# Performance work log

Hardware: AMD Instinct MI355X
Metric: run time of the kernel (lower is better)

## Reference

```python
import jax, jax.numpy as jnp
import numpy as np

X_DIM = 64
Y_DIM = 64
U_DIM = 64
BATCH = 32
SEQ_LEN = 2048
DT = 1.0 / 1024.0
EPS = 1e-4


def setup_inputs() -> dict:
    key = jax.random.key(0)
    k_y, k_a, k_c = jax.random.split(key, 3)
    y = jax.random.normal(k_y, (BATCH, SEQ_LEN, Y_DIM), dtype=jnp.float32)
    # parameters, matching the module's initialization (small noise added to A/C for generality)
    A = jnp.diag(-0.01 * (jnp.arange(X_DIM, dtype=jnp.float32) + 1.0)) \
        + 0.001 * jax.random.normal(k_a, (X_DIM, X_DIM), dtype=jnp.float32)
    B = jnp.eye(X_DIM, U_DIM, dtype=jnp.float32) * 0.1
    C = 0.1 * jax.random.normal(k_c, (Y_DIM, X_DIM), dtype=jnp.float32)
    L_Q = jnp.eye(X_DIM, dtype=jnp.float32) * 0.316
    L_R = jnp.eye(U_DIM, dtype=jnp.float32) * 0.316
    L_V = jnp.eye(Y_DIM, dtype=jnp.float32)
    L_Q_proc = jnp.eye(X_DIM, dtype=jnp.float32) * 0.1
    x0_mean = jnp.zeros((X_DIM,), dtype=jnp.float32)
    P0 = jnp.eye(X_DIM, dtype=jnp.float32) * 0.1
    return {"y": y, "A": A, "B": B, "C": C, "L_Q": L_Q, "L_R": L_R,
            "L_V": L_V, "L_Q_proc": L_Q_proc, "x0_mean": x0_mean, "P0": P0}


def _riccati_step(S, H, n):
    # Euler step of the augmented Hamiltonian flow; P = V @ U^{-1}
    S_new = S + DT * (H @ S)
    U, V = S_new[:n], S_new[n:]
    X = V @ jnp.linalg.inv(U)
    return X, S_new


def _forward(y, A, B, C, L_Q, L_R, L_V, L_Q_proc, x0_mean, P0):
    n = A.shape[0]
    u_dim = B.shape[1]
    y_dim = C.shape[0]
    batch, seq_len, _ = y.shape

    Q = L_Q @ L_Q.T
    R = L_R @ L_R.T
    V = L_V @ L_V.T
    Q_proc = L_Q_proc @ L_Q_proc.T

    # normalize observations (torch.std is unbiased -> ddof=1)
    y_mean = y.mean(axis=(0, 1), keepdims=True)
    y_std = y.std(axis=(0, 1), keepdims=True, ddof=1)
    yn = (y - y_mean) / (y_std + EPS)

    # --- LQR Riccati recursion: P_seq, K_seq (sequential scan over time) ---
    R_inv_reg = jnp.linalg.inv(R + EPS * jnp.eye(u_dim, dtype=R.dtype))
    H_care = jnp.block([[A, -B @ jnp.linalg.inv(R) @ B.T],
                        [-Q, -A.T]])  # augmented Hamiltonian (2n, 2n)

    def lqr_step(S, _):
        X, S_new = _riccati_step(S, H_care, n)
        P = 0.5 * (X + X.T)
        K = R_inv_reg @ (B.T @ P)  # (u_dim, n)
        return S_new, (P, K)

    S0 = jnp.concatenate([jnp.eye(n, dtype=Q.dtype), Q], axis=0)  # P0 = Q
    _, (P_seq, K_seq) = jax.lax.scan(lqr_step, S0, None, length=seq_len)

    # --- Kalman filter (sequential scan, data-dependent per-step linear algebra) ---
    V_reg = V + EPS * jnp.eye(y_dim, dtype=V.dtype)
    V_chol = jnp.linalg.cholesky(V_reg)
    log_det_V = 2.0 * jnp.sum(jnp.log(jnp.diagonal(V_chol)))
    Z = jnp.zeros((n, n), dtype=A.dtype)
    LOG_2PI = jnp.log(2.0 * jnp.pi).astype(A.dtype)

    def kf_step(carry, inp):
        x_t, S, ll = carry
        K_t, y_t = inp  # (u_dim, n), (batch, y_dim)
        A_eff = A - B @ K_t
        x_pred = x_t + DT * (x_t @ A_eff.T)  # (batch, n)
        H_t = jnp.block([[A_eff, Q_proc], [Z, -A_eff.T]])
        P_new, S = _riccati_step(S, H_t, n)
        P_pred = 0.5 * (P_new + P_new.T)
        residual = y_t - x_pred @ C.T  # (batch, y_dim)
        CtP = C @ P_pred  # (y_dim, n)
        Sm = CtP @ C.T + V
        S_inv = jnp.linalg.inv(Sm + EPS * jnp.eye(y_dim, dtype=Sm.dtype))
        Kg = CtP.T @ S_inv  # (n, y_dim)
        x_new = x_pred + residual @ Kg.T
        quad = jnp.sum(residual * (residual @ S_inv.T))  # sum_b r^T S_inv r
        ll = ll - 0.5 * (quad + log_det_V + y_dim * LOG_2PI)
        return (x_new, S, ll), x_new

    S0_kf = jnp.concatenate([jnp.eye(n, dtype=P0.dtype), P0], axis=0)
    x0 = jnp.broadcast_to(x0_mean, (batch, n))
    y_t_major = jnp.swapaxes(yn, 0, 1)  # (T, B, y_dim)
    (_, _, ll), x_filt_t = jax.lax.scan(kf_step, (x0, S0_kf, jnp.float32(0.0)),
                                        (K_seq, y_t_major))
    x_filt = jnp.swapaxes(x_filt_t, 0, 1)  # (B, T, n)
    log_likelihood = ll / seq_len

    # controls, prediction, quadratic costs (fully vectorized)
    u_seq = -jnp.einsum('tux,btx->btu', K_seq, x_filt)
    y_pred = x_filt @ C.T
    x_cost = jnp.einsum('btx,xz,btz->b', x_filt, Q, x_filt)
    u_cost = jnp.einsum('btu,uv,btv->b', u_seq, R, u_seq)
    control_cost = jnp.mean(x_cost + u_cost)
    return log_likelihood, control_cost, x_filt, u_seq, y_pred, yn


def reference(y, A, B, C, L_Q, L_R, L_V, L_Q_proc, x0_mean, P0):
    return _forward(y, A, B, C, L_Q, L_R, L_V, L_Q_proc, x0_mean, P0)
```

## Files before the change

kernel.cpp:

```cpp
#include <hip/hip_runtime.h>
#include <math.h>

#define XD 64
#define SEQL 2048
#define NB 32
#define DT_C  (1.0f/1024.0f)
#define EPS_C 1e-4f
#define LD 68
#define PLD 136
#define LOG2PI 1.8378770664093453f
#define CHUNK 16
#define NCH 128

#define OFF_PARTIAL 0u
#define OFF_MEAN    32768u
#define OFF_STD     32832u
#define OFF_Q       32896u
#define OFF_R       36992u
#define OFF_VM      41088u
#define OFF_QP      45184u
#define OFF_RIREG   49280u
#define OFF_LOGDET  53376u
#define OFF_CHAIN   53440u
#define OFF_POW     250048u
#define OFF_BOUNDS  1298624u
#define OFF_K       1568960u
#define OFF_AEFF    9957568u
#define OFF_UV      18346176u
#define OFF_G       35123392u
#define OFF_B       43512000u
#define OFF_OPS2    47706304u
#define OFF_OPS3G   50852032u
#define OFF_OPS3B   51900608u
#define OFF_SB2     52424896u
#define OFF_XB      53473472u
#define OFF_QUAD    53735616u
#define OFF_COST    53737664u

#define OOFF_XF 2
#define OOFF_U  4194306
#define OOFF_YP 8388610
#define OOFF_YN 12582914

template<int KD>
__device__ __forceinline__ void mmNN(int t, float* __restrict__ out, int ldo,
    const float* __restrict__ A, int lda, const float* __restrict__ B, int ldb,
    const float* __restrict__ addC = nullptr, int ldc = 0, float alpha = 1.0f)
{
  const int r0 = (t >> 4) << 2, c0 = (t & 15) << 2;
  float acc[4][4] = {};
  for (int k = 0; k < KD; k += 4) {
    float a_[4][4];
    #pragma unroll
    for (int i = 0; i < 4; ++i) {
      const float4 x = *(const float4*)&A[(r0+i)*lda + k];
      a_[i][0]=x.x; a_[i][1]=x.y; a_[i][2]=x.z; a_[i][3]=x.w;
    }
    #pragma unroll
    for (int kk = 0; kk < 4; ++kk) {
      const float4 bv = *(const float4*)&B[(k+kk)*ldb + c0];
      #pragma unroll
      for (int i = 0; i < 4; ++i) {
        const float a = a_[i][kk];
        acc[i][0] += a*bv.x; acc[i][1] += a*bv.y; acc[i][2] += a*bv.z; acc[i][3] += a*bv.w;
      }
    }
  }
  #pragma unroll
  for (int i = 0; i < 4; ++i)
    #pragma unroll
    for (int j = 0; j < 4; ++j) {
      float v = alpha*acc[i][j];
      if (addC) v += addC[(r0+i)*ldc + (c0+j)];
      out[(r0+i)*ldo + (c0+j)] = v;
    }
}

template<int KD>
__device__ __forceinline__ void mmTA(int t, float* __restrict__ out, int ldo,
    const float* __restrict__ A, int lda, const float* __restrict__ B, int ldb,
    const float* __restrict__ addC = nullptr, int ldc = 0, float alpha = 1.0f)
{
  const int r0 = (t >> 4) << 2, c0 = (t & 15) << 2;
  float acc[4][4] = {};
  for (int k = 0; k < KD; k += 4) {
    #pragma unroll
    for (int kk = 0; kk < 4; ++kk) {
      const float4 av4 = *(const float4*)&A[(k+kk)*lda + r0];
      const float4 bv4 = *(const float4*)&B[(k+kk)*ldb + c0];
      const float av[4] = {av4.x, av4.y, av4.z, av4.w};
      const float bv[4] = {bv4.x, bv4.y, bv4.z, bv4.w};
      #pragma unroll
      for (int i = 0; i < 4; ++i)
        #pragma unroll
        for (int j = 0; j < 4; ++j)
          acc[i][j] += av[i]*bv[j];
    }
  }
  #pragma unroll
  for (int i = 0; i < 4; ++i)
    #pragma unroll
    for (int j = 0; j < 4; ++j) {
      float v = alpha*acc[i][j];
      if (addC) v += addC[(r0+i)*ldc + (c0+j)];
      out[(r0+i)*ldo + (c0+j)] = v;
    }
}

template<int KD>
__device__ __forceinline__ void mmTB(int t, float* __restrict__ out, int ldo,
    const float* __restrict__ A, int lda, const float* __restrict__ B, int ldb,
    const float* __restrict__ addC = nullptr, int ldc = 0, float alpha = 1.0f)
{
  const int r0 = (t >> 4) << 2, c0 = (t & 15) << 2;
  float acc[4][4] = {};
  for (int k = 0; k < KD; k += 4) {
    float a_[4][4], b_[4][4];
    #pragma unroll
    for (int i = 0; i < 4; ++i) {
      const float4 x = *(const float4*)&A[(r0+i)*lda + k];
      a_[i][0]=x.x; a_[i][1]=x.y; a_[i][2]=x.z; a_[i][3]=x.w;
    }
    #pragma unroll
    for (int j = 0; j < 4; ++j) {
      const float4 x = *(const float4*)&B[(c0+j)*ldb + k];
      b_[j][0]=x.x; b_[j][1]=x.y; b_[j][2]=x.z; b_[j][3]=x.w;
    }
    #pragma unroll
    for (int i = 0; i < 4; ++i)
      #pragma unroll
      for (int j = 0; j < 4; ++j)
        acc[i][j] += a_[i][0]*b_[j][0] + a_[i][1]*b_[j][1] + a_[i][2]*b_[j][2] + a_[i][3]*b_[j][3];
  }
  #pragma unroll
  for (int i = 0; i < 4; ++i)
    #pragma unroll
    for (int j = 0; j < 4; ++j) {
      float v = alpha*acc[i][j];
      if (addC) v += addC[(r0+i)*ldc + (c0+j)];
      out[(r0+i)*ldo + (c0+j)] = v;
    }
}

template<int KD>
__device__ __forceinline__ void mm32NN(int t, float* __restrict__ out, int ldo,
    const float* __restrict__ A, int lda, const float* __restrict__ B, int ldb,
    const float* __restrict__ addC = nullptr, int ldc = 0, float alpha = 1.0f)
{
  const int r0 = (t >> 4) << 1, c0 = (t & 15) << 2;
  float acc[2][4] = {};
  for (int k = 0; k < KD; k += 4) {
    float a_[2][4];
    #pragma unroll
    for (int i = 0; i < 2; ++i) {
      const float4 x = *(const float4*)&A[(r0+i)*lda + k];
      a_[i][0]=x.x; a_[i][1]=x.y; a_[i][2]=x.z; a_[i][3]=x.w;
    }
    #pragma unroll
    for (int kk = 0; kk < 4; ++kk) {
      const float4 bv = *(const float4*)&B[(k+kk)*ldb + c0];
      #pragma unroll
      for (int i = 0; i < 2; ++i) {
        const float a = a_[i][kk];
        acc[i][0] += a*bv.x; acc[i][1] += a*bv.y; acc[i][2] += a*bv.z; acc[i][3] += a*bv.w;
      }
    }
  }
  #pragma unroll
  for (int i = 0; i < 2; ++i)
    #pragma unroll
    for (int j = 0; j < 4; ++j) {
      float v = alpha*acc[i][j];
      if (addC) v += addC[(r0+i)*ldc + (c0+j)];
      out[(r0+i)*ldo + (c0+j)] = v;
    }
}

template<int KD>
__device__ __forceinline__ void mm32TB(int t, float* __restrict__ out, int ldo,
    const float* __restrict__ A, int lda, const float* __restrict__ B, int ldb,
    const float* __restrict__ addC = nullptr, int ldc = 0, float alpha = 1.0f)
{
  const int r0 = (t >> 4) << 1, c0 = (t & 15) << 2;
  float acc[2][4] = {};
  for (int k = 0; k < KD; k += 4) {
    float a_[2][4], b_[4][4];
    #pragma unroll
    for (int i = 0; i < 2; ++i) {
      const float4 x = *(const float4*)&A[(r0+i)*lda + k];
      a_[i][0]=x.x; a_[i][1]=x.y; a_[i][2]=x.z; a_[i][3]=x.w;
    }
    #pragma unroll
    for (int j = 0; j < 4; ++j) {
      const float4 x = *(const float4*)&B[(c0+j)*ldb + k];
      b_[j][0]=x.x; b_[j][1]=x.y; b_[j][2]=x.z; b_[j][3]=x.w;
    }
    #pragma unroll
    for (int i = 0; i < 2; ++i)
      #pragma unroll
      for (int j = 0; j < 4; ++j)
        acc[i][j] += a_[i][0]*b_[j][0] + a_[i][1]*b_[j][1] + a_[i][2]*b_[j][2] + a_[i][3]*b_[j][3];
  }
  #pragma unroll
  for (int i = 0; i < 2; ++i)
    #pragma unroll
    for (int j = 0; j < 4; ++j) {
      float v = alpha*acc[i][j];
      if (addC) v += addC[(r0+i)*ldc + (c0+j)];
      out[(r0+i)*ldo + (c0+j)] = v;
    }
}

__device__ __forceinline__ void gj64(int t, float* __restrict__ Am, float* __restrict__ R)
{
  const int r = t >> 2;
  const int c0 = (t & 3) << 4;
  for (int k = 0; k < 64; ++k) {
    __syncthreads();
    const float pv = Am[k*LD + k];
    const float f = Am[r*LD + k] / pv;
    if (r != k) {
      #pragma unroll
      for (int c = 0; c < 16; c += 4) {
        float4 ak = *(const float4*)&Am[k*LD + c0 + c];
        float4 ar = *(float4*)&Am[r*LD + c0 + c];
        ar.x -= f*ak.x; ar.y -= f*ak.y; ar.z -= f*ak.z; ar.w -= f*ak.w;
        *(float4*)&Am[r*LD + c0 + c] = ar;
        float4 rk = *(const float4*)&R[k*LD + c0 + c];
        float4 rr = *(float4*)&R[r*LD + c0 + c];
        rr.x -= f*rk.x; rr.y -= f*rk.y; rr.z -= f*rk.z; rr.w -= f*rk.w;
        *(float4*)&R[r*LD + c0 + c] = rr;
      }
    }
  }
  __syncthreads();
  const float dinv = 1.0f / Am[r*LD + r];
  #pragma unroll
  for (int c = 0; c < 16; c += 4) {
    float4 rr = *(float4*)&R[r*LD + c0 + c];
    rr.x *= dinv; rr.y *= dinv; rr.z *= dinv; rr.w *= dinv;
    *(float4*)&R[r*LD + c0 + c] = rr;
  }
  __syncthreads();
}

__device__ __forceinline__ void gjb8(int t, float* __restrict__ Am, float* __restrict__ R,
                                     float* __restrict__ pnl, float* __restrict__ w8)
{
  const int r  = t >> 2;
  const int c0 = (t & 3) << 4;
  const int j2 = t >> 5;
  const int cc = (t & 31) << 2;
  for (int kb = 0; kb < 8; ++kb) {
    const int K = kb << 3;
    __syncthreads();
    if (t < 64) {
      const int i = t >> 3, j = t & 7;
      float a = Am[(K+i)*LD + K + j];
      float w = (i == j) ? 1.0f : 0.0f;
      #pragma unroll
      for (int p = 0; p < 8; ++p) {
        const float pv  = __shfl(a, p*8 + p, 64);
        const float aip = __shfl(a, i*8 + p, 64);
        const float apj = __shfl(a, p*8 + j, 64);
        const float wpj = __shfl(w, p*8 + j, 64);
        const float fi  = aip / pv;
        if (i == p) { a = a / pv; w = w / pv; }
        else        { a -= fi * apj; w -= fi * wpj; }
      }
      w8[t] = w;
    }
    __syncthreads();
    {
      const int c4 = cc & 63;
      const float* srcB = (cc < 64) ? Am : R;
      const int off = (cc < 64) ? 0 : 68;
      float4 acc = make_float4(0.f, 0.f, 0.f, 0.f);
      #pragma unroll
      for (int m = 0; m < 8; ++m) {
        const float wv = w8[j2*8 + m];
        const float4 rv = *(const float4*)&srcB[(K+m)*LD + c4];
        acc.x += wv*rv.x; acc.y += wv*rv.y; acc.z += wv*rv.z; acc.w += wv*rv.w;
      }
      *(float4*)&pnl[j2*PLD + off + c4] = acc;
    }
    __syncthreads();
    {
      const float4 f0 = *(const float4*)&Am[r*LD + K];
      const float4 f1 = *(const float4*)&Am[r*LD + K + 4];
      const float fj[8] = {f0.x, f0.y, f0.z, f0.w, f1.x, f1.y, f1.z, f1.w};
      const bool inK = ((unsigned)(r - K)) < 8u;
      #pragma unroll
      for (int c = 0; c < 16; c += 4) {
        const int cab = c0 + c;
        if (cab >= K + 8) {
          float4 v;
          if (inK) {
            v = *(const float4*)&pnl[(r-K)*PLD + cab];
          } else {
            v = *(float4*)&Am[r*LD + cab];
            #pragma unroll
            for (int j = 0; j < 8; ++j) {
              const float4 p4 = *(const float4*)&pnl[j*PLD + cab];
              v.x -= fj[j]*p4.x; v.y -= fj[j]*p4.y; v.z -= fj[j]*p4.z; v.w -= fj[j]*p4.w;
            }
          }
          *(float4*)&Am[r*LD + cab] = v;
        }
      }
      #pragma unroll
      for (int c = 0; c < 16; c += 4) {
        const int cab = c0 + c;
        float4 v;
        if (inK) {
          v = *(const float4*)&pnl[(r-K)*PLD + 68 + cab];
        } else {
          v = *(float4*)&R[r*LD + cab];
          #pragma unroll
          for (int j = 0; j < 8; ++j) {
            const float4 p4 = *(const float4*)&pnl[j*PLD + 68 + cab];
            v.x -= fj[j]*p4.x; v.y -= fj[j]*p4.y; v.z -= fj[j]*p4.z; v.w -= fj[j]*p4.w;
          }
        }
        *(float4*)&R[r*LD + cab] = v;
      }
    }
  }
  __syncthreads();
}


__global__ __launch_bounds__(256) void k_stats(const float* __restrict__ y, float* __restrict__ ws)
{
  __shared__ float sbuf[4][128];
  const int t = threadIdx.x, blk = blockIdx.x;
  const int d = t & 63, g = t >> 6;
  float s = 0.f, s2 = 0.f;
  for (int r = g; r < 256; r += 4) {
    const float v = y[(size_t)(blk*256 + r)*64 + d];
    s += v; s2 += v*v;
  }
  sbuf[g][d] = s; sbuf[g][64+d] = s2;
  __syncthreads();
  if (t < 128) ws[OFF_PARTIAL + (size_t)blk*128 + t] = sbuf[0][t]+sbuf[1][t]+sbuf[2][t]+sbuf[3][t];
}

__global__ __launch_bounds__(256) void k_setup(
    const float* __restrict__ A, const float* __restrict__ Bi,
    const float* __restrict__ LQ, const float* __restrict__ LR,
    const float* __restrict__ LV, const float* __restrict__ LQp,
    float* __restrict__ ws)
{
  __shared__ float b1[64*LD], b2[64*LD], b3[64*LD], b4[64*LD], bQ[64*LD];
  __shared__ float sred[128];
  const int t = threadIdx.x;

  if (t < 128) {
    float acc = 0.f;
    for (int p = 0; p < 256; ++p) acc += ws[OFF_PARTIAL + (size_t)p*128 + t];
    sred[t] = acc;
  }
  __syncthreads();
  if (t < 64) {
    const float mean = sred[t] * (1.0f/65536.0f);
    const float var = (sred[64+t] - 65536.0f*mean*mean) * (1.0f/65535.0f);
    ws[OFF_MEAN + t] = mean;
    ws[OFF_STD + t] = sqrtf(var);
  }

  mmTB<64>(t, bQ, LD, LQ, 64, LQ, 64);
  mmTB<64>(t, b3, LD, LR, 64, LR, 64);
  mmTB<64>(t, ws+OFF_VM, 64, LV, 64, LV, 64);
  mmTB<64>(t, ws+OFF_QP, 64, LQp, 64, LQp, 64);
  __syncthreads();
  for (int idx = t; idx < 4096; idx += 256) {
    const int r = idx>>6, c = idx&63;
    ws[OFF_Q + idx] = bQ[r*LD+c];
    ws[OFF_R + idx] = b3[r*LD+c];
    b1[r*LD+c] = b3[r*LD+c] + ((r==c)?EPS_C:0.f);
    b2[r*LD+c] = (r==c)?1.f:0.f;
  }
  gj64(t, b1, b2);
  for (int idx = t; idx < 4096; idx += 256) ws[OFF_RIREG + idx] = b2[(idx>>6)*LD+(idx&63)];
  __syncthreads();
  for (int idx = t; idx < 4096; idx += 256) {
    const int r = idx>>6, c = idx&63;
    b1[r*LD+c] = b3[r*LD+c];
    b2[r*LD+c] = (r==c)?1.f:0.f;
  }
  gj64(t, b1, b2);
  mmTB<64>(t, b3, LD, b2, LD, Bi, 64);
  __syncthreads();
  mmNN<64>(t, b4, LD, Bi, 64, b3, LD);
  mmTB<64>(t, b1, LD, LV, 64, LV, 64);
  __syncthreads();
  if (t < 64) b1[t*LD+t] += EPS_C;
  {
    const int r = t >> 2, c0 = (t & 3) << 4;
    float lsum = 0.f;
    for (int k = 0; k < 64; ++k) {
      __syncthreads();
      const float pv = b1[k*LD+k];
      lsum += logf(pv);
      const float f = b1[r*LD+k] / pv;
      if (r != k) {
        #pragma unroll
        for (int c = 0; c < 16; c += 4) {
          float4 ak = *(const float4*)&b1[k*LD+c0+c];
          float4 ar = *(float4*)&b1[r*LD+c0+c];
          ar.x -= f*ak.x; ar.y -= f*ak.y; ar.z -= f*ak.z; ar.w -= f*ak.w;
          *(float4*)&b1[r*LD+c0+c] = ar;
        }
      }
    }
    if (t == 0) ws[OFF_LOGDET] = lsum;
  }
  __syncthreads();
  float* M0 = ws + OFF_CHAIN;
  for (int idx = t; idx < 16384; idx += 256) {
    const int i = idx >> 7, j = idx & 127;
    float v;
    if (i < 64) v = (j < 64) ? (((i==j)?1.f:0.f) + DT_C*A[i*64+j]) : (-DT_C*b4[i*LD + (j-64)]);
    else        v = (j < 64) ? (-DT_C*bQ[(i-64)*LD + j]) : (((i==j)?1.f:0.f) - DT_C*A[(j-64)*64 + (i-64)]);
    M0[idx] = v;
  }
  for (int idx = t; idx < 16384; idx += 256) {
    const int i = idx >> 7, j = idx & 127;
    ws[OFF_POW + idx] = (i==j)?1.f:0.f;
  }
  for (int idx = t; idx < 8192; idx += 256) {
    const int i = idx >> 6, j = idx & 63;
    ws[OFF_BOUNDS + idx] = (i < 64) ? ((i==j)?1.f:0.f) : bQ[(i-64)*LD + j];
  }
}

__global__ __launch_bounds__(256) void k_yn(const float* __restrict__ y, const float* __restrict__ ws, float* __restrict__ out)
{
  const size_t i0 = ((size_t)blockIdx.x*256 + threadIdx.x)*4;
  const int d = (int)(i0 & 63);
  const float4 v = *(const float4*)&y[i0];
  const float4 m = *(const float4*)&ws[OFF_MEAN + d];
  const float4 s = *(const float4*)&ws[OFF_STD + d];
  float* o = out + OOFF_YN + i0;
  o[0] = (v.x - m.x)/(s.x + EPS_C);
  o[1] = (v.y - m.y)/(s.y + EPS_C);
  o[2] = (v.z - m.z)/(s.z + EPS_C);
  o[3] = (v.w - m.w)/(s.w + EPS_C);
}

__global__ __launch_bounds__(256) void k_sq(const float* __restrict__ src, float* __restrict__ dst)
{
  const int t = threadIdx.x;
  const int r = blockIdx.x*8 + (t >> 5);
  const int c0 = (t & 31) << 2;
  float acc[4] = {0.f,0.f,0.f,0.f};
  for (int k = 0; k < 128; k += 4) {
    const float4 a4 = *(const float4*)&src[r*128 + k];
    const float av[4] = {a4.x, a4.y, a4.z, a4.w};
    #pragma unroll
    for (int kk = 0; kk < 4; ++kk) {
      const float4 bv = *(const float4*)&src[(k+kk)*128 + c0];
      acc[0] += av[kk]*bv.x; acc[1] += av[kk]*bv.y; acc[2] += av[kk]*bv.z; acc[3] += av[kk]*bv.w;
    }
  }
  float4 o; o.x=acc[0]; o.y=acc[1]; o.z=acc[2]; o.w=acc[3];
  *(float4*)&dst[r*128 + c0] = o;
}

__global__ __launch_bounds__(256) void k_pow(const float* __restrict__ chainj, float* __restrict__ powt, int level)
{
  const int i = blockIdx.x >> 2, sub = blockIdx.x & 3;
  const float* Bm = powt + (size_t)i*16384;
  float* D = powt + (size_t)(i + (1<<level))*16384;
  const int t = threadIdx.x;
  const int r0 = sub*32 + ((t >> 4) << 1);
  const int c0 = (t & 15) << 3;
  float acc[2][8] = {};
  for (int k = 0; k < 128; k += 4) {
    float a_[2][4];
    {
      const float4 x = *(const float4*)&chainj[r0*128 + k];
      a_[0][0]=x.x; a_[0][1]=x.y; a_[0][2]=x.z; a_[0][3]=x.w;
      const float4 y2 = *(const float4*)&chainj[(r0+1)*128 + k];
      a_[1][0]=y2.x; a_[1][1]=y2.y; a_[1][2]=y2.z; a_[1][3]=y2.w;
    }
    #pragma unroll
    for (int kk = 0; kk < 4; ++kk) {
      const float4 b0 = *(const float4*)&Bm[(k+kk)*128 + c0];
      const float4 b1v = *(const float4*)&Bm[(k+kk)*128 + c0 + 4];
      #pragma unroll
      for (int i2 = 0; i2 < 2; ++i2) {
        const float a = a_[i2][kk];
        acc[i2][0] += a*b0.x; acc[i2][1] += a*b0.y; acc[i2][2] += a*b0.z; acc[i2][3] += a*b0.w;
        acc[i2][4] += a*b1v.x; acc[i2][5] += a*b1v.y; acc[i2][6] += a*b1v.z; acc[i2][7] += a*b1v.w;
      }
    }
  }
  #pragma unroll
  for (int i2 = 0; i2 < 2; ++i2)
    #pragma unroll
    for (int j = 0; j < 8; ++j)
      D[(r0+i2)*128 + c0 + j] = acc[i2][j];
}

__global__ __launch_bounds__(256) void k_boundsk(const float* __restrict__ chainp, float* __restrict__ ws, int level)
{
  const int kb = blockIdx.x >> 1, sub = blockIdx.x & 1;
  const int dsti = kb + (1 << level);
  if (dsti > 32) return;
  const float* S = ws + OFF_BOUNDS + (size_t)kb*8192;
  float* D = ws + OFF_BOUNDS + (size_t)dsti*8192;
  const int t = threadIdx.x;
  const int r0 = sub*64 + ((t >> 4) << 2);
  const int c0 = (t & 15) << 2;
  float acc[4][4] = {};
  for (int k = 0; k < 128; k += 4) {
    float a_[4][4];
    #pragma unroll
    for (int i = 0; i < 4; ++i) {
      const float4 x = *(const float4*)&chainp[(r0+i)*128 + k];
      a_[i][0]=x.x; a_[i][1]=x.y; a_[i][2]=x.z; a_[i][3]=x.w;
    }
    #pragma unroll
    for (int kk = 0; kk < 4; ++kk) {
      const float4 bv = *(const float4*)&S[(k+kk)*64 + c0];
      #pragma unroll
      for (int i = 0; i < 4; ++i) {
        const float a = a_[i][kk];
        acc[i][0] += a*bv.x; acc[i][1] += a*bv.y; acc[i][2] += a*bv.z; acc[i][3] += a*bv.w;
      }
    }
  }
  #pragma unroll
  for (int i = 0; i < 4; ++i)
    #pragma unroll
    for (int j = 0; j < 4; ++j)
      D[(r0+i)*64 + c0 + j] = acc[i][j];
}

__global__ __launch_bounds__(256) void k_lqr(const float* __restrict__ Ain, const float* __restrict__ Bin, float* __restrict__ ws)
{
  __shared__ float b1[64*LD], b2[64*LD], b3[64*LD];
  __shared__ float pnl[8*PLD], w8[64];
  const int t = threadIdx.x, tt = blockIdx.x;
  const int tp1 = tt + 1, kc = tp1 >> 6, rr = tp1 & 63;
  const float* Mr = ws + OFF_POW + (size_t)rr*16384;
  const float* SB = ws + OFF_BOUNDS + (size_t)kc*8192;
  mmNN<128>(t, b1, LD, Mr, 128, SB, 64);
  mmNN<128>(t, b3, LD, Mr + 8192, 128, SB, 64);
  for (int idx = t; idx < 4096; idx += 256) {
    const int r = idx>>6, c = idx&63;
    b2[r*LD+c] = (r==c)?1.f:0.f;
  }
  gjb8(t, b1, b2, pnl, w8);
  mmNN<64>(t, b1, LD, b3, LD, b2, LD);
  __syncthreads();
  for (int idx = t; idx < 4096; idx += 256) {
    const int r = idx>>6, c = idx&63;
    b3[r*LD+c] = 0.5f*(b1[r*LD+c] + b1[c*LD+r]);
  }
  __syncthreads();
  mmTA<64>(t, b1, LD, Bin, 64, b3, LD);
  __syncthreads();
  mmNN<64>(t, b2, LD, ws+OFF_RIREG, 64, b1, LD);
  __syncthreads();
  float* Kout = ws + OFF_K + (size_t)tt*4096;
  for (int idx = t; idx < 4096; idx += 256) Kout[idx] = b2[(idx>>6)*LD+(idx&63)];
  mmNN<64>(t, b1, LD, Bin, 64, b2, LD);
  __syncthreads();
  float* Ae = ws + OFF_AEFF + (size_t)tt*4096;
  for (int idx = t; idx < 4096; idx += 256) Ae[idx] = Ain[idx] - b1[(idx>>6)*LD+(idx&63)];
}

__global__ __launch_bounds__(1024) void k_ops2(const float* __restrict__ ws_aeff, const float* __restrict__ ws_qp, float* __restrict__ dstE)
{
  __shared__ float E[64*LD], W[64*LD], F[64*LD], T1[64*LD], T2[64*LD], T3[64*LD], T4[64*LD];
  const int t = threadIdx.x, c = blockIdx.x, g = t >> 8, tl = t & 255;
  for (int idx = t; idx < 4096; idx += 1024) {
    const int r = idx>>6, cc = idx&63; const float id = (r==cc)?1.f:0.f;
    E[r*LD+cc] = id; W[r*LD+cc] = 0.f; F[r*LD+cc] = id;
  }
  __syncthreads();
  for (int s = 0; s < CHUNK; ++s) {
    const float* Ae = ws_aeff + ((size_t)c*CHUNK + s)*4096;
    if (g == 0)      mmNN<64>(tl, T1, LD, Ae, 64, E, LD);
    else if (g == 1) mmNN<64>(tl, T2, LD, Ae, 64, W, LD);
    else if (g == 2) mmNN<64>(tl, T3, LD, ws_qp, 64, F, LD);
    else             mmTA<64>(tl, T4, LD, Ae, 64, F, LD);
    __syncthreads();
    for (int idx = t; idx < 4096; idx += 1024) {
      const int p = (idx>>6)*LD + (idx&63);
      E[p] += DT_C*T1[p];
      W[p] += DT_C*(T2[p] + T3[p]);
      F[p] -= DT_C*T4[p];
    }
    __syncthreads();
  }
  float* dst = dstE + (size_t)c*12288;
  for (int idx = t; idx < 4096; idx += 1024) {
    const int p = (idx>>6)*LD + (idx&63);
    dst[idx] = E[p]; dst[4096+idx] = W[p]; dst[8192+idx] = F[p];
  }
}

__global__ __launch_bounds__(1024) void k_scan2(const float* __restrict__ src, float* __restrict__ dst, int s)
{
  __shared__ float t1[64*LD], t2[64*LD];
  const int i = blockIdx.x, t = threadIdx.x, g = t>>8, tl = t&255;
  const float* si = src + (size_t)i*12288;
  float* di = dst + (size_t)i*12288;
  if (i < s) {
    for (int idx = t; idx < 12288; idx += 1024) di[idx] = si[idx];
    return;
  }
  const float* sj = src + (size_t)(i-s)*12288;
  if (g == 0)      mmNN<64>(tl, di, 64, si, 64, sj, 64);
  else if (g == 1) mmNN<64>(tl, t1, LD, si, 64, sj+4096, 64);
  else if (g == 2) mmNN<64>(tl, t2, LD, si+4096, 64, sj+8192, 64);
  else             mmNN<64>(tl, di+8192, 64, si+8192, 64, sj+8192, 64);
  __syncthreads();
  for (int idx = t; idx < 4096; idx += 1024) {
    const int p = (idx>>6)*LD + (idx&63);
    di[4096+idx] = t1[p] + t2[p];
  }
}

__global__ __launch_bounds__(256) void k_sb2(const float* __restrict__ phi, const float* __restrict__ P0, float* __restrict__ ws)
{
  const int c = blockIdx.x, t = threadIdx.x;
  float* D = ws + OFF_SB2 + (size_t)c*8192;
  if (c == 0) {
    for (int idx = t; idx < 4096; idx += 256) {
      const int r = idx>>6, cc = idx&63;
      D[idx] = (r==cc)?1.f:0.f;
      D[4096+idx] = P0[idx];
    }
    return;
  }
  const float* ph = phi + (size_t)(c-1)*12288;
  mmNN<64>(t, D, 64, ph+4096, 64, P0, 64, ph, 64);
  mmNN<64>(t, D+4096, 64, ph+8192, 64, P0, 64);
}

__global__ __launch_bounds__(1024) void k_uvwalk(const float* __restrict__ ws_aeff, const float* __restrict__ ws_qp,
    const float* __restrict__ ws_sb2, float* __restrict__ ws_uv)
{
  __shared__ float U[64*LD], V[64*LD], T1[64*LD], T2[64*LD], T3[64*LD];
  const int c = blockIdx.x, t = threadIdx.x, g = t>>8, tl = t&255;
  const float* S = ws_sb2 + (size_t)c*8192;
  for (int idx = t; idx < 4096; idx += 1024) {
    const int p = (idx>>6)*LD + (idx&63);
    U[p] = S[idx]; V[p] = S[4096+idx];
  }
  __syncthreads();
  for (int s = 0; s < CHUNK; ++s) {
    const size_t tt = (size_t)c*CHUNK + s;
    const float* Ae = ws_aeff + tt*4096;
    if (g == 0)      mmNN<64>(tl, T1, LD, Ae, 64, U, LD);
    else if (g == 1) mmNN<64>(tl, T2, LD, ws_qp, 64, V, LD);
    else if (g == 2) mmTA<64>(tl, T3, LD, Ae, 64, V, LD);
    __syncthreads();
    float* O = ws_uv + tt*8192;
    for (int idx = t; idx < 4096; idx += 1024) {
      const int p = (idx>>6)*LD + (idx&63);
      const float un = U[p] + DT_C*(T1[p] + T2[p]);
      const float vn = V[p] - DT_C*T3[p];
      U[p] = un; V[p] = vn;
      O[idx] = un; O[4096+idx] = vn;
    }
    __syncthreads();
  }
}

__global__ __launch_bounds__(256) void k_kfper(const float* __restrict__ Cin, float* __restrict__ ws)
{
  __shared__ float b1[64*LD], b2[64*LD], b3[64*LD];
  __shared__ float pnl[8*PLD], w8[64];
  const int t = threadIdx.x, tt = blockIdx.x;
  float* base = ws + OFF_UV + (size_t)tt*8192;
  for (int idx = t; idx < 4096; idx += 256) {
    const int r = idx>>6, c = idx&63;
    b1[r*LD+c] = base[idx];
    b2[r*LD+c] = (r==c)?1.f:0.f;
  }
  gjb8(t, b1, b2, pnl, w8);
  mmNN<64>(t, b3, LD, base+4096, 64, b2, LD);
  __syncthreads();
  for (int idx = t; idx < 4096; idx += 256) {
    const int r = idx>>6, c = idx&63;
    b1[r*LD+c] = 0.5f*(b3[r*LD+c] + b3[c*LD+r]);
  }
  __syncthreads();
  mmNN<64>(t, b3, LD, Cin, 64, b1, LD);
  __syncthreads();
  mmTB<64>(t, b2, LD, b3, LD, Cin, 64, ws+OFF_VM, 64);
  __syncthreads();
  if (t < 64) b2[t*LD+t] += EPS_C;
  for (int idx = t; idx < 4096; idx += 256) {
    const int r = idx>>6, c = idx&63;
    b1[r*LD+c] = (r==c)?1.f:0.f;
  }
  gjb8(t, b2, b1, pnl, w8);
  for (int idx = t; idx < 4096; idx += 256) base[4096+idx] = b1[(idx>>6)*LD+(idx&63)];
  mmTA<64>(t, b2, LD, b3, LD, b1, LD);
  __syncthreads();
  for (int idx = t; idx < 4096; idx += 256) base[idx] = b2[(idx>>6)*LD+(idx&63)];
  mmNN<64>(t, b3, LD, b2, LD, Cin, 64);
  __syncthreads();
  const float* Ae = ws + OFF_AEFF + (size_t)tt*4096;
  float* Gg = ws + OFF_G + (size_t)tt*4096;
  {
    const int r0 = (t>>4)<<2, cg0 = (t&15)<<2;
    float acc[4][4] = {};
    for (int k = 0; k < 64; k += 4) {
      float a_[4][4];
      #pragma unroll
      for (int kk = 0; kk < 4; ++kk) {
        const float4 x = *(const float4*)&Ae[(k+kk)*64 + r0];
        a_[kk][0]=x.x; a_[kk][1]=x.y; a_[kk][2]=x.z; a_[kk][3]=x.w;
      }
      float yv[4][4];
      #pragma unroll
      for (int j = 0; j < 4; ++j) {
        const float4 z4 = *(const float4*)&b3[(cg0+j)*LD + k];
        yv[j][0] = -z4.x; yv[j][1] = -z4.y; yv[j][2] = -z4.z; yv[j][3] = -z4.w;
        const int dk = (cg0+j) - k;
        if (dk >= 0 && dk < 4) yv[j][dk] += 1.0f;
      }
      #pragma unroll
      for (int kk = 0; kk < 4; ++kk)
        #pragma unroll
        for (int i = 0; i < 4; ++i) {
          const float a = a_[kk][i];
          #pragma unroll
          for (int j = 0; j < 4; ++j) acc[i][j] += a * yv[j][kk];
        }
    }
    #pragma unroll
    for (int i = 0; i < 4; ++i)
      #pragma unroll
      for (int j = 0; j < 4; ++j) {
        const int rw = r0+i, cw = cg0+j;
        const float Yij = ((rw==cw)?1.f:0.f) - b3[cw*LD + rw];
        Gg[rw*64+cw] = Yij + DT_C*acc[i][j];
      }
  }
}

__global__ __launch_bounds__(256) void k_bvec(const float* __restrict__ outyn, float* __restrict__ ws)
{
  __shared__ float y32[NB*LD];
  const int tt = blockIdx.x, t = threadIdx.x;
  for (int idx = t; idx < 2048; idx += 256) {
    const int i = idx>>6, d = idx&63;
    y32[i*LD+d] = outyn[(size_t)i*131072 + (size_t)tt*64 + d];
  }
  __syncthreads();
  mm32TB<64>(t, ws + OFF_B + (size_t)tt*2048, 64, y32, LD, ws + OFF_UV + (size_t)tt*8192, 64);
}

__global__ __launch_bounds__(1024) void k_ops3(const float* __restrict__ ws_g, const float* __restrict__ ws_b,
    float* __restrict__ dG, float* __restrict__ dB)
{
  __shared__ float Gc[64*LD], TG[64*LD], bc[NB*LD], Tb[NB*LD];
  const int t = threadIdx.x, c = blockIdx.x, g = t >> 8, tl = t & 255;
  for (int idx = t; idx < 4096; idx += 1024) {
    const int r = idx>>6, cc = idx&63;
    Gc[r*LD+cc] = (r==cc)?1.f:0.f;
  }
  for (int idx = t; idx < 2048; idx += 1024) bc[(idx>>6)*LD+(idx&63)] = 0.f;
  __syncthreads();
  for (int s = 0; s < CHUNK; ++s) {
    const size_t tt = (size_t)c*CHUNK + s;
    const float* Gt = ws_g + tt*4096;
    if (g == 0)      mmNN<64>(tl, TG, LD, Gc, LD, Gt, 64);
    else if (g == 1) mm32NN<64>(tl, Tb, LD, bc, LD, Gt, 64);
    __syncthreads();
    for (int idx = t; idx < 4096; idx += 1024) {
      const int p = (idx>>6)*LD + (idx&63);
      Gc[p] = TG[p];
    }
    const float* bt = ws_b + tt*2048;
    for (int idx = t; idx < 2048; idx += 1024) {
      const int p = (idx>>6)*LD + (idx&63);
      bc[p] = Tb[p] + bt[idx];
    }
    __syncthreads();
  }
  for (int idx = t; idx < 4096; idx += 1024) dG[(size_t)c*4096 + idx] = Gc[(idx>>6)*LD+(idx&63)];
  for (int idx = t; idx < 2048; idx += 1024) dB[(size_t)c*2048 + idx] = bc[(idx>>6)*LD+(idx&63)];
}

__global__ __launch_bounds__(512) void k_scan3(const float* __restrict__ sG, const float* __restrict__ sB,
    float* __restrict__ dG, float* __restrict__ dB, int s)
{
  const int i = blockIdx.x, t = threadIdx.x, g = t>>8, tl = t&255;
  if (i < s) {
    for (int idx = t; idx < 4096; idx += 512) dG[(size_t)i*4096+idx] = sG[(size_t)i*4096+idx];
    for (int idx = t; idx < 2048; idx += 512) dB[(size_t)i*2048+idx] = sB[(size_t)i*2048+idx];
    return;
  }
  const float* Ge = sG + (size_t)(i-s)*4096;
  const float* Gl = sG + (size_t)i*4096;
  if (g == 0) mmNN<64>(tl, dG + (size_t)i*4096, 64, Ge, 64, Gl, 64);
  else        mm32NN<64>(tl, dB + (size_t)i*2048, 64, sB + (size_t)(i-s)*2048, 64, Gl, 64,
                         sB + (size_t)i*2048, 64);
}

__global__ __launch_bounds__(256) void k_xb(const float* __restrict__ phiG, const float* __restrict__ phiB,
    const float* __restrict__ x0, float* __restrict__ ws)
{
  __shared__ float v[64];
  const int c = blockIdx.x, t = threadIdx.x;
  float* D = ws + OFF_XB + (size_t)c*2048;
  if (c == 0) {
    for (int idx = t; idx < 2048; idx += 256) D[idx] = x0[idx&63];
    return;
  }
  const float* G = phiG + (size_t)(c-1)*4096;
  const float* b = phiB + (size_t)(c-1)*2048;
  if (t < 64) {
    float acc = 0.f;
    for (int k = 0; k < 64; ++k) acc += x0[k]*G[k*64 + t];
    v[t] = acc;
  }
  __syncthreads();
  for (int idx = t; idx < 2048; idx += 256) D[idx] = v[idx&63] + b[idx];
}

__global__ __launch_bounds__(256) void k_xwalk(const float* __restrict__ ws_g, const float* __restrict__ ws_b,
    const float* __restrict__ ws_xb, float* __restrict__ outx)
{
  __shared__ float x[NB*LD], xn[NB*LD];
  const int c = blockIdx.x, t = threadIdx.x;
  const float* X0 = ws_xb + (size_t)c*2048;
  for (int idx = t; idx < 2048; idx += 256) x[(idx>>6)*LD+(idx&63)] = X0[idx];
  __syncthreads();
  for (int s = 0; s < CHUNK; ++s) {
    const size_t tt = (size_t)c*CHUNK + s;
    mm32NN<64>(t, xn, LD, x, LD, ws_g + tt*4096, 64, ws_b + tt*2048, 64);
    __syncthreads();
    for (int idx = t; idx < 2048; idx += 256) {
      const int i = idx>>6, d = idx&63;
      const float val = xn[i*LD+d];
      x[i*LD+d] = val;
      outx[(size_t)i*131072 + tt*64 + d] = val;
    }
    __syncthreads();
  }
}

__global__ __launch_bounds__(256) void k_final(const float* __restrict__ Cin, const float* __restrict__ x0,
    const float* __restrict__ outx, const float* __restrict__ outyn,
    float* __restrict__ outu, float* __restrict__ outyp, float* __restrict__ ws)
{
  __shared__ float xc[NB*LD], z[NB*LD], t1[NB*LD], t2[NB*LD];
  __shared__ float red4[4];
  const int tt = blockIdx.x, t = threadIdx.x;
  for (int idx = t; idx < 2048; idx += 256) {
    const int i = idx>>6, d = idx&63;
    xc[i*LD+d] = outx[(size_t)i*131072 + (size_t)tt*64 + d];
    z[i*LD+d]  = (tt == 0) ? x0[d] : outx[(size_t)i*131072 + (size_t)(tt-1)*64 + d];
  }
  __syncthreads();
  mm32TB<64>(t, t1, LD, xc, LD, ws + OFF_K + (size_t)tt*4096, 64, nullptr, 0, -1.0f);
  mm32TB<64>(t, t2, LD, xc, LD, Cin, 64);
  __syncthreads();
  for (int idx = t; idx < 2048; idx += 256) {
    const int i = idx>>6, d = idx&63;
    outu[(size_t)i*131072 + (size_t)tt*64 + d]  = t1[i*LD+d];
    outyp[(size_t)i*131072 + (size_t)tt*64 + d] = t2[i*LD+d];
  }
  __syncthreads();
  mm32NN<64>(t, t2, LD, xc, LD, ws + OFF_Q, 64);
  __syncthreads();
  const int i_ = t >> 3, lane8 = t & 7;
  float cpart = 0.f;
  for (int d = lane8; d < 64; d += 8) cpart += t2[i_*LD+d]*xc[i_*LD+d];
  __syncthreads();
  mm32NN<64>(t, t2, LD, t1, LD, ws + OFF_R, 64);
  __syncthreads();
  for (int d = lane8; d < 64; d += 8) cpart += t2[i_*LD+d]*t1[i_*LD+d];
  cpart += __shfl_down(cpart, 4, 8);
  cpart += __shfl_down(cpart, 2, 8);
  cpart += __shfl_down(cpart, 1, 8);
  if (lane8 == 0) ws[OFF_COST + (size_t)tt*32 + i_] = cpart;
  __syncthreads();
  mm32TB<64>(t, t2, LD, z, LD, ws + OFF_AEFF + (size_t)tt*4096, 64, z, LD, DT_C);
  __syncthreads();
  mm32TB<64>(t, t1, LD, t2, LD, Cin, 64, outyn + (size_t)tt*64, 131072, -1.0f);
  __syncthreads();
  mm32TB<64>(t, z, LD, t1, LD, ws + OFF_UV + (size_t)tt*8192 + 4096, 64);
  __syncthreads();
  float q = 0.f;
  for (int idx = t; idx < 2048; idx += 256) {
    const int p = (idx>>6)*LD + (idx&63);
    q += t1[p]*z[p];
  }
  q += __shfl_down(q, 32); q += __shfl_down(q, 16); q += __shfl_down(q, 8);
  q += __shfl_down(q, 4);  q += __shfl_down(q, 2);  q += __shfl_down(q, 1);
  if ((t & 63) == 0) red4[t>>6] = q;
  __syncthreads();
  if (t == 0) ws[OFF_QUAD + tt] = red4[0]+red4[1]+red4[2]+red4[3];
}

__global__ __launch_bounds__(256) void k_scalars(const float* __restrict__ ws, float* __restrict__ out)
{
  __shared__ float red[256];
  const int t = threadIdx.x;
  float q = 0.f;
  for (int i = t; i < 2048; i += 256) q += ws[OFF_QUAD + i];
  red[t] = q;
  __syncthreads();
  for (int s = 128; s > 0; s >>= 1) { if (t < s) red[t] += red[t+s]; __syncthreads(); }
  const float quadsum = red[0];
  __syncthreads();
  {
    const int b = t & 31, chunk = t >> 5;
    float a = 0.f;
    for (int j = 0; j < 256; ++j) a += ws[OFF_COST + (size_t)(chunk*256 + j)*32 + b];
    red[t] = a;
  }
  __syncthreads();
  if (t < 32) {
    float a = 0.f;
    for (int ch = 0; ch < 8; ++ch) a += red[ch*32 + t];
    red[t] = a;
  }
  __syncthreads();
  if (t == 0) {
    float cc = 0.f;
    for (int b = 0; b < 32; ++b) cc += red[b];
    out[1] = cc / 32.0f;
    const float ld = ws[OFF_LOGDET];
    out[0] = -0.5f*(quadsum + 2048.0f*(ld + 64.0f*LOG2PI)) / 2048.0f;
  }
}

extern "C" void kernel_launch(void* const* d_in, const int* in_sizes, int n_in,
                              void* d_out, int out_size, void* d_ws, size_t ws_size,
                              hipStream_t stream)
{
  (void)in_sizes; (void)n_in; (void)out_size; (void)ws_size;
  const float* y   = (const float*)d_in[0];
  const float* A   = (const float*)d_in[1];
  const float* Bi  = (const float*)d_in[2];
  const float* C   = (const float*)d_in[3];
  const float* LQ  = (const float*)d_in[4];
  const float* LR  = (const float*)d_in[5];
  const float* LV  = (const float*)d_in[6];
  const float* LQp = (const float*)d_in[7];
  const float* x0  = (const float*)d_in[8];
  const float* P0  = (const float*)d_in[9];
  float* out = (float*)d_out;
  float* ws  = (float*)d_ws;

  k_stats<<<256, 256, 0, stream>>>(y, ws);
  k_setup<<<1, 256, 0, stream>>>(A, Bi, LQ, LR, LV, LQp, ws);
  k_yn<<<4096, 256, 0, stream>>>(y, ws, out);

  for (int j = 1; j <= 11; ++j)
    k_sq<<<16, 256, 0, stream>>>(ws + OFF_CHAIN + (size_t)(j-1)*16384, ws + OFF_CHAIN + (size_t)j*16384);
  for (int j = 0; j <= 5; ++j)
    k_pow<<<4 << j, 256, 0, stream>>>(ws + OFF_CHAIN + (size_t)j*16384, ws + OFF_POW, j);
  for (int j = 0; j <= 5; ++j)
    k_boundsk<<<2 << j, 256, 0, stream>>>(ws + OFF_CHAIN + (size_t)(6+j)*16384, ws, j);

  k_lqr<<<2048, 256, 0, stream>>>(A, Bi, ws);

  k_ops2<<<NCH, 1024, 0, stream>>>(ws + OFF_AEFF, ws + OFF_QP, ws + OFF_OPS2);
  {
    float* pa = ws + OFF_OPS2;
    float* pb = pa + (size_t)NCH*12288;
    float* src = pa; float* dst = pb;
    for (int s = 1; s < NCH; s <<= 1) {
      k_scan2<<<NCH, 1024, 0, stream>>>(src, dst, s);
      float* tmp = src; src = dst; dst = tmp;
    }
    k_sb2<<<NCH, 256, 0, stream>>>(src, P0, ws);
  }
  k_uvwalk<<<NCH, 1024, 0, stream>>>(ws + OFF_AEFF, ws + OFF_QP, ws + OFF_SB2, ws + OFF_UV);
  k_kfper<<<2048, 256, 0, stream>>>(C, ws);

  k_bvec<<<2048, 256, 0, stream>>>(out + OOFF_YN, ws);
  k_ops3<<<NCH, 1024, 0, stream>>>(ws + OFF_G, ws + OFF_B, ws + OFF_OPS3G, ws + OFF_OPS3B);
  {
    float* ga = ws + OFF_OPS3G; float* gb = ga + (size_t)NCH*4096;
    float* ba = ws + OFF_OPS3B; float* bb = ba + (size_t)NCH*2048;
    float *gs = ga, *gd = gb, *bs = ba, *bd = bb;
    for (int s = 1; s < NCH; s <<= 1) {
      k_scan3<<<NCH, 512, 0, stream>>>(gs, bs, gd, bd, s);
      float* t1p = gs; gs = gd; gd = t1p;
      float* t2p = bs; bs = bd; bd = t2p;
    }
    k_xb<<<NCH, 256, 0, stream>>>(gs, bs, x0, ws);
  }
  k_xwalk<<<NCH, 256, 0, stream>>>(ws + OFF_G, ws + OFF_B, ws + OFF_XB, out + OOFF_XF);

  k_final<<<2048, 256, 0, stream>>>(C, x0, out + OOFF_XF, out + OOFF_YN, out + OOFF_U, out + OOFF_YP, ws);
  k_scalars<<<1, 256, 0, stream>>>(ws, out);
}
```

Before: 2.542 ms.

## Halve scan chunk size, fuse symmetrization into matmuls, merge bvec into kfper

Cuts CHUNK from 16 to 8 and doubles the number of chunks, so the sequential per-chunk walks get shorter while the parallel scan needs one more level. The explicit P=(X+X^T)/2 symmetrization passes are folded into new symmetric-operand matmuls in k_lqr and k_kfper. B*R_inv is precomputed so Aeff is written straight to global memory in one fused matmul. The separate k_bvec kernel is merged into k_kfper, and the OPS2 buffer now aliases the UV region to make room. In exchange the aliasing adds a risk of overlapping live workspace data.

```diff
diff --git a/kernel.cpp b/kernel.cpp
--- a/kernel.cpp
+++ b/kernel.cpp
@@ -9,8 +9,8 @@
 #define LD 68
 #define PLD 136
 #define LOG2PI 1.8378770664093453f
-#define CHUNK 16
-#define NCH 128
+#define CHUNK 8
+#define NCH 256
 
 #define OFF_PARTIAL 0u
 #define OFF_MEAN    32768u
@@ -29,13 +29,14 @@
 #define OFF_UV      18346176u
 #define OFF_G       35123392u
 #define OFF_B       43512000u
-#define OFF_OPS2    47706304u
-#define OFF_OPS3G   50852032u
-#define OFF_OPS3B   51900608u
-#define OFF_SB2     52424896u
-#define OFF_XB      53473472u
-#define OFF_QUAD    53735616u
-#define OFF_COST    53737664u
+#define OFF_OPS2    OFF_UV
+#define OFF_OPS3G   47706304u
+#define OFF_OPS3B   49803456u
+#define OFF_SB2     50852032u
+#define OFF_XB      52949184u
+#define OFF_QUAD    53473472u
+#define OFF_COST    53475520u
+#define OFF_BRI     53541056u
 
 #define OOFF_XF 2
 #define OOFF_U  4194306
@@ -142,6 +143,88 @@
     }
 }
 
+__device__ __forceinline__ void mmNNsym(int t, float* __restrict__ out, int ldo,
+    const float* __restrict__ A, int lda, const float* __restrict__ X,
+    const float* __restrict__ addC = nullptr, int ldc = 0)
+{
+  const int r0 = (t >> 4) << 2, c0 = (t & 15) << 2;
+  float acc[4][4] = {};
+  for (int k = 0; k < 64; k += 4) {
+    float a_[4][4];
+    #pragma unroll
+    for (int i = 0; i < 4; ++i) {
+      const float4 x = *(const float4*)&A[(r0+i)*lda + k];
+      a_[i][0]=x.x; a_[i][1]=x.y; a_[i][2]=x.z; a_[i][3]=x.w;
+    }
+    float xr[4][4], xc[4][4];
+    #pragma unroll
+    for (int kk = 0; kk < 4; ++kk) {
+      const float4 x = *(const float4*)&X[(k+kk)*LD + c0];
+      xr[kk][0]=x.x; xr[kk][1]=x.y; xr[kk][2]=x.z; xr[kk][3]=x.w;
+    }
+    #pragma unroll
+    for (int j = 0; j < 4; ++j) {
+      const float4 x = *(const float4*)&X[(c0+j)*LD + k];
+      xc[j][0]=x.x; xc[j][1]=x.y; xc[j][2]=x.z; xc[j][3]=x.w;
+    }
+    #pragma unroll
+    for (int kk = 0; kk < 4; ++kk)
+      #pragma unroll
+      for (int j = 0; j < 4; ++j) {
+        const float s = xr[kk][j] + xc[j][kk];
+        #pragma unroll
+        for (int i = 0; i < 4; ++i) acc[i][j] += a_[i][kk]*s;
+      }
+  }
+  #pragma unroll
+  for (int i = 0; i < 4; ++i)
+    #pragma unroll
+    for (int j = 0; j < 4; ++j) {
+      float v = 0.5f*acc[i][j];
+      if (addC) v += addC[(r0+i)*ldc + (c0+j)];
+      out[(r0+i)*ldo + (c0+j)] = v;
+    }
+}
+
+__device__ __forceinline__ void mmTAsym(int t, float* __restrict__ out, int ldo,
+    const float* __restrict__ B, int ldb, const float* __restrict__ X)
+{
+  const int r0 = (t >> 4) << 2, c0 = (t & 15) << 2;
+  float acc[4][4] = {};
+  for (int k = 0; k < 64; k += 4) {
+    float av[4][4];
+    #pragma unroll
+    for (int kk = 0; kk < 4; ++kk) {
+      const float4 x = *(const float4*)&B[(k+kk)*ldb + r0];
+      av[kk][0]=x.x; av[kk][1]=x.y; av[kk][2]=x.z; av[kk][3]=x.w;
+    }
+    float xr[4][4], xc[4][4];
+    #pragma unroll
+    for (int kk = 0; kk < 4; ++kk) {
+      const float4 x = *(const float4*)&X[(k+kk)*LD + c0];
+      xr[kk][0]=x.x; xr[kk][1]=x.y; xr[kk][2]=x.z; xr[kk][3]=x.w;
+    }
+    #pragma unroll
+    for (int j = 0; j < 4; ++j) {
+      const float4 x = *(const float4*)&X[(c0+j)*LD + k];
+      xc[j][0]=x.x; xc[j][1]=x.y; xc[j][2]=x.z; xc[j][3]=x.w;
+    }
+    #pragma unroll
+    for (int kk = 0; kk < 4; ++kk)
+      #pragma unroll
+      for (int j = 0; j < 4; ++j) {
+        const float s = xr[kk][j] + xc[j][kk];
+        #pragma unroll
+        for (int i = 0; i < 4; ++i) acc[i][j] += av[kk][i]*s;
+      }
+  }
+  #pragma unroll
+  for (int i = 0; i < 4; ++i)
+    #pragma unroll
+    for (int j = 0; j < 4; ++j)
+      out[(r0+i)*ldo + (c0+j)] = 0.5f*acc[i][j];
+}
+
 template<int KD>
 __device__ __forceinline__ void mm32NN(int t, float* __restrict__ out, int ldo,
     const float* __restrict__ A, int lda, const float* __restrict__ B, int ldb,
@@ -178,8 +261,8 @@
 
 template<int KD>
 __device__ __forceinline__ void mm32TB(int t, float* __restrict__ out, int ldo,
-    const float* __restrict__ A, int lda, const float* __restrict__ B, int ldb,
-    const float* __restrict__ addC = nullptr, int ldc = 0, float alpha = 1.0f)
+    const float* __restrict__ A, size_t lda, const float* __restrict__ B, int ldb,
+    const float* __restrict__ addC = nullptr, size_t ldc = 0, float alpha = 1.0f)
 {
   const int r0 = (t >> 4) << 1, c0 = (t & 15) << 2;
   float acc[2][4] = {};
@@ -187,7 +270,7 @@
     float a_[2][4], b_[4][4];
     #pragma unroll
     for (int i = 0; i < 2; ++i) {
-      const float4 x = *(const float4*)&A[(r0+i)*lda + k];
+      const float4 x = *(const float4*)&A[(size_t)(r0+i)*lda + k];
       a_[i][0]=x.x; a_[i][1]=x.y; a_[i][2]=x.z; a_[i][3]=x.w;
     }
     #pragma unroll
@@ -206,7 +289,7 @@
     #pragma unroll
     for (int j = 0; j < 4; ++j) {
       float v = alpha*acc[i][j];
-      if (addC) v += addC[(r0+i)*ldc + (c0+j)];
+      if (addC) v += addC[(size_t)(r0+i)*ldc + (c0+j)];
       out[(r0+i)*ldo + (c0+j)] = v;
     }
 }
@@ -381,7 +464,12 @@
     b2[r*LD+c] = (r==c)?1.f:0.f;
   }
   gj64(t, b1, b2);
-  for (int idx = t; idx < 4096; idx += 256) ws[OFF_RIREG + idx] = b2[(idx>>6)*LD+(idx&63)];
+  mmNN<64>(t, b4, LD, Bi, 64, b2, LD);
+  __syncthreads();
+  for (int idx = t; idx < 4096; idx += 256) {
+    ws[OFF_RIREG + idx] = b2[(idx>>6)*LD+(idx&63)];
+    ws[OFF_BRI + idx]   = b4[(idx>>6)*LD+(idx&63)];
+  }
   __syncthreads();
   for (int idx = t; idx < 4096; idx += 256) {
     const int r = idx>>6, c = idx&63;
@@ -555,21 +643,14 @@
   gjb8(t, b1, b2, pnl, w8);
   mmNN<64>(t, b1, LD, b3, LD, b2, LD);
   __syncthreads();
-  for (int idx = t; idx < 4096; idx += 256) {
-    const int r = idx>>6, c = idx&63;
-    b3[r*LD+c] = 0.5f*(b1[r*LD+c] + b1[c*LD+r]);
-  }
-  __syncthreads();
-  mmTA<64>(t, b1, LD, Bin, 64, b3, LD);
-  __syncthreads();
-  mmNN<64>(t, b2, LD, ws+OFF_RIREG, 64, b1, LD);
+  mmTAsym(t, b3, LD, Bin, 64, b1);
+  __syncthreads();
+  mmNN<64>(t, b2, LD, ws+OFF_RIREG, 64, b3, LD);
+  mmNN<64>(t, ws + OFF_AEFF + (size_t)tt*4096, 64,
+           ws + OFF_BRI, 64, b3, LD, Ain, 64, -1.0f);
   __syncthreads();
   float* Kout = ws + OFF_K + (size_t)tt*4096;
   for (int idx = t; idx < 4096; idx += 256) Kout[idx] = b2[(idx>>6)*LD+(idx&63)];
-  mmNN<64>(t, b1, LD, Bin, 64, b2, LD);
-  __syncthreads();
-  float* Ae = ws + OFF_AEFF + (size_t)tt*4096;
-  for (int idx = t; idx < 4096; idx += 256) Ae[idx] = Ain[idx] - b1[(idx>>6)*LD+(idx&63)];
 }
 
 __global__ __launch_bounds__(1024) void k_ops2(const float* __restrict__ ws_aeff, const float* __restrict__ ws_qp, float* __restrict__ dstE)
@@ -672,7 +753,7 @@
   }
 }
 
-__global__ __launch_bounds__(256) void k_kfper(const float* __restrict__ Cin, float* __restrict__ ws)
+__global__ __launch_bounds__(256) void k_kfper(const float* __restrict__ Cin, const float* __restrict__ outyn, float* __restrict__ ws)
 {
   __shared__ float b1[64*LD], b2[64*LD], b3[64*LD];
   __shared__ float pnl[8*PLD], w8[64];
@@ -681,25 +762,21 @@
   for (int idx = t; idx < 4096; idx += 256) {
     const int r = idx>>6, c = idx&63;
     b1[r*LD+c] = base[idx];
+    b3[r*LD+c] = base[4096+idx];
     b2[r*LD+c] = (r==c)?1.f:0.f;
   }
   gjb8(t, b1, b2, pnl, w8);
-  mmNN<64>(t, b3, LD, base+4096, 64, b2, LD);
-  __syncthreads();
-  for (int idx = t; idx < 4096; idx += 256) {
-    const int r = idx>>6, c = idx&63;
-    b1[r*LD+c] = 0.5f*(b3[r*LD+c] + b3[c*LD+r]);
-  }
-  __syncthreads();
-  mmNN<64>(t, b3, LD, Cin, 64, b1, LD);
+  mmNN<64>(t, b1, LD, b3, LD, b2, LD);
+  __syncthreads();
+  mmNNsym(t, b3, LD, Cin, 64, b1);
   __syncthreads();
   mmTB<64>(t, b2, LD, b3, LD, Cin, 64, ws+OFF_VM, 64);
-  __syncthreads();
-  if (t < 64) b2[t*LD+t] += EPS_C;
   for (int idx = t; idx < 4096; idx += 256) {
     const int r = idx>>6, c = idx&63;
     b1[r*LD+c] = (r==c)?1.f:0.f;
   }
+  __syncthreads();
+  if (t < 64) b2[t*LD+t] += EPS_C;
   gjb8(t, b2, b1, pnl, w8);
   for (int idx = t; idx < 4096; idx += 256) base[4096+idx] = b1[(idx>>6)*LD+(idx&63)];
   mmTA<64>(t, b2, LD, b3, LD, b1, LD);
@@ -742,21 +819,15 @@
       for (int j = 0; j < 4; ++j) {
         const int rw = r0+i, cw = cg0+j;
         const float Yij = ((rw==cw)?1.f:0.f) - b3[cw*LD + rw];
-        Gg[rw*64+cw] = Yij + DT_C*acc[i][j];
-      }
-  }
-}
-
-__global__ __launch_bounds__(256) void k_bvec(const float* __restrict__ outyn, float* __restrict__ ws)
-{
-  __shared__ float y32[NB*LD];
-  const int tt = blockIdx.x, t = threadIdx.x;
-  for (int idx = t; idx < 2048; idx += 256) {
-    const int i = idx>>6, d = idx&63;
-    y32[i*LD+d] = outyn[(size_t)i*131072 + (size_t)tt*64 + d];
-  }
-  __syncthreads();
-  mm32TB<64>(t, ws + OFF_B + (size_t)tt*2048, 64, y32, LD, ws + OFF_UV + (size_t)tt*8192, 64);
+        b1[rw*LD+cw] = Yij + DT_C*acc[i][j];
+      }
+  }
+  __syncthreads();
+  for (int idx = t; idx < 4096; idx += 256) Gg[idx] = b1[(idx>>6)*LD+(idx&63)];
+  mm32TB<64>(t, b3, LD, outyn + (size_t)tt*64, (size_t)131072, b2, LD);
+  __syncthreads();
+  float* Bout = ws + OFF_B + (size_t)tt*2048;
+  for (int idx = t; idx < 2048; idx += 256) Bout[idx] = b3[(idx>>6)*LD+(idx&63)];
 }
 
 __global__ __launch_bounds__(1024) void k_ops3(const float* __restrict__ ws_g, const float* __restrict__ ws_b,
@@ -888,7 +959,7 @@
   __syncthreads();
   mm32TB<64>(t, t2, LD, z, LD, ws + OFF_AEFF + (size_t)tt*4096, 64, z, LD, DT_C);
   __syncthreads();
-  mm32TB<64>(t, t1, LD, t2, LD, Cin, 64, outyn + (size_t)tt*64, 131072, -1.0f);
+  mm32TB<64>(t, t1, LD, t2, LD, Cin, 64, outyn + (size_t)tt*64, (size_t)131072, -1.0f);
   __syncthreads();
   mm32TB<64>(t, z, LD, t1, LD, ws + OFF_UV + (size_t)tt*8192 + 4096, 64);
   __syncthreads();
@@ -980,9 +1051,8 @@
     k_sb2<<<NCH, 256, 0, stream>>>(src, P0, ws);
   }
   k_uvwalk<<<NCH, 1024, 0, stream>>>(ws + OFF_AEFF, ws + OFF_QP, ws + OFF_SB2, ws + OFF_UV);
-  k_kfper<<<2048, 256, 0, stream>>>(C, ws);
-
-  k_bvec<<<2048, 256, 0, stream>>>(out + OOFF_YN, ws);
+  k_kfper<<<2048, 256, 0, stream>>>(C, out + OOFF_YN, ws);
+
   k_ops3<<<NCH, 1024, 0, stream>>>(ws + OFF_G, ws + OFF_B, ws + OFF_OPS3G, ws + OFF_OPS3B);
   {
     float* ga = ws + OFF_OPS3G; float* gb = ga + (size_t)NCH*4096;
```

Result: no change. 2.515 ms (-1.1%).
